# Kernel tuning notes

Measured on AMD Instinct MI355X. Metric: run time of the kernel, lower is better.

Reference implementation:

```python
import jax, jax.numpy as jnp
import numpy as np

B, T, D = 2, 1024, 2048      # batch, seq, model dim
E, F, K = 64, 512, 4          # n_experts, expert hidden, top-k
S, HS = 2, 512 * 4            # shared experts, shared hidden = expert_dim * topk


def setup_inputs() -> dict:
    key = jax.random.key(0)
    ks = jax.random.split(key, 9)
    s = 0.02
    f32 = jnp.float32
    return {
        "x": jax.random.normal(ks[0], (B, T, D), f32),
        "router_w": jax.random.normal(ks[1], (D, E), f32) * s,
        "router_bias": jnp.zeros((E,), f32),
        "wg": jax.random.normal(ks[2], (E, D, F), f32) * s,
        "wu": jax.random.normal(ks[3], (E, D, F), f32) * s,
        "wd": jax.random.normal(ks[4], (E, F, D), f32) * s,
        "swg": jax.random.normal(ks[5], (S, D, HS), f32) * s,
        "swu": jax.random.normal(ks[6], (S, D, HS), f32) * s,
        "swd": jax.random.normal(ks[7], (S, HS, D), f32) * s,
    }


def reference(x, router_w, router_bias, wg, wu, wd, swg, swu, swd):
    b, t, d = x.shape
    flat = x.reshape(b * t, d)                      # [N, D]
    n = flat.shape[0]

    # Router: softmax scores, top-k selection on (logits + bias)
    logits = flat @ router_w                         # [N, E]
    scores = jax.nn.softmax(logits, axis=-1)
    _, topk_idx = jax.lax.top_k(logits + router_bias, K)          # [N, K]
    topk_scores = jnp.take_along_axis(scores, topk_idx, axis=-1)  # [N, K]
    topk_scores = topk_scores / topk_scores.sum(axis=-1, keepdims=True)

    # Dense combine weights: w[n, e] = normalized score if expert e selected else 0
    comb = jnp.zeros((n, E), dtype=flat.dtype).at[
        jnp.arange(n)[:, None], topk_idx].set(topk_scores)        # [N, E]

    # Routed experts (SwiGLU), computed densely and masked by combine weights
    g = jax.nn.silu(jnp.einsum('nd,edf->nef', flat, wg))          # [N, E, F]
    u = jnp.einsum('nd,edf->nef', flat, wu)                       # [N, E, F]
    routed = jnp.einsum('ne,nef,efd->nd', comb, g * u, wd)        # [N, D]

    # Shared experts (always active, summed)
    sg = jax.nn.silu(jnp.einsum('nd,sdh->nsh', flat, swg))        # [N, S, HS]
    su = jnp.einsum('nd,sdh->nsh', flat, swu)
    shared = jnp.einsum('nsh,shd->nd', sg * su, swd)              # [N, D]

    return (routed + shared).reshape(b, t, d)
```

## Files before the change

kernel.cpp:

```cpp
#include <hip/hip_runtime.h>
#include <hip/hip_bf16.h>

typedef __bf16 bf16x8 __attribute__((ext_vector_type(8)));
typedef float f32x4 __attribute__((ext_vector_type(4)));
typedef unsigned short u16x4 __attribute__((ext_vector_type(4)));
typedef unsigned short u16x8 __attribute__((ext_vector_type(8)));

#define DEVI __device__ __forceinline__

constexpr int N_TOK = 2048;
constexpr int DIM   = 2048;
constexpr int NEXP  = 64;
constexpr int FDIM  = 512;
constexpr int TOPK  = 4;
constexpr int NSH   = 2;
constexpr int HSH   = 2048;

constexpr int BM = 128, BN = 128, BK = 64, KS = 8;

DEVI unsigned short f2b(float f) {
  union { float fv; unsigned u; } v; v.fv = f;
  unsigned r = v.u + 0x7fffu + ((v.u >> 16) & 1u);
  return (unsigned short)(r >> 16);
}
DEVI float b2f(unsigned short h) {
  union { unsigned u; float f; } v; v.u = ((unsigned)h) << 16;
  return v.f;
}
DEVI void gll16(const void* g, void* l) {
  __builtin_amdgcn_global_load_lds((const __attribute__((address_space(1))) unsigned*)g,
                                   (__attribute__((address_space(3))) unsigned*)l, 16, 0, 0);
}

__global__ void cvt_x_kernel(const float* __restrict__ x, unsigned short* __restrict__ xb) {
  const size_t i = ((size_t)blockIdx.x * 256 + threadIdx.x) * 8;
  const float4 a = *reinterpret_cast<const float4*>(x + i);
  const float4 b = *reinterpret_cast<const float4*>(x + i + 4);
  u16x8 o;
  o[0] = f2b(a.x); o[1] = f2b(a.y); o[2] = f2b(a.z); o[3] = f2b(a.w);
  o[4] = f2b(b.x); o[5] = f2b(b.y); o[6] = f2b(b.z); o[7] = f2b(b.w);
  *reinterpret_cast<u16x8*>(xb + i) = o;
}

__global__ __launch_bounds__(256)
void tr_shared_kernel(const float* __restrict__ swu, const float* __restrict__ swg,
                      const float* __restrict__ swd, unsigned short* __restrict__ swuT,
                      unsigned short* __restrict__ swgT, unsigned short* __restrict__ swdT) {
  __shared__ float Lf[64][68];
  const int tid = threadIdx.x;
  const int r0 = blockIdx.x * 64, c0 = blockIdx.y * 64;
  const int z = blockIdx.z, mat = z >> 1;
  const size_t soff = (size_t)(z & 1) * DIM * HSH;
  const float* in = (mat == 0 ? swu : mat == 1 ? swg : swd) + soff;
  unsigned short* ot = (mat == 0 ? swuT : mat == 1 ? swgT : swdT) + soff;
  #pragma unroll
  for (int j = 0; j < 4; ++j) {
    const int idx = j * 1024 + tid * 4;
    const int row = idx >> 6, col = idx & 63;
    const float4 v = *reinterpret_cast<const float4*>(in + (size_t)(r0 + row) * 2048 + c0 + col);
    *reinterpret_cast<float4*>(&Lf[row][col]) = v;
  }
  __syncthreads();
  #pragma unroll
  for (int j = 0; j < 4; ++j) {
    const int idx = j * 1024 + tid * 4;
    const int orow = idx >> 6, ocol = idx & 63;
    u16x4 o;
    o[0] = f2b(Lf[ocol][orow]);     o[1] = f2b(Lf[ocol + 1][orow]);
    o[2] = f2b(Lf[ocol + 2][orow]); o[3] = f2b(Lf[ocol + 3][orow]);
    *reinterpret_cast<u16x4*>(ot + (size_t)(c0 + orow) * 2048 + r0 + ocol) = o;
  }
}

__global__ void router_kernel(const float* __restrict__ x, const float* __restrict__ rw,
                              const float* __restrict__ rb, int* __restrict__ cnt,
                              int* __restrict__ listTok, float* __restrict__ listW) {
  const int lane = threadIdx.x & 63;
  const int wave = threadIdx.x >> 6;
  const int tokBase = blockIdx.x * 8 + wave * 2;
  const float* __restrict__ xr0 = x + (size_t)tokBase * DIM;
  const float* __restrict__ xr1 = xr0 + DIM;
  float acc0 = 0.f, acc1 = 0.f;
  for (int d = 0; d < DIM; ++d) {
    const float r = rw[(size_t)d * NEXP + lane];
    acc0 = fmaf(xr0[d], r, acc0);
    acc1 = fmaf(xr1[d], r, acc1);
  }
  const float bias = rb[lane];
  #pragma unroll
  for (int t = 0; t < 2; ++t) {
    const float v = (t == 0) ? acc0 : acc1;
    const int token = tokBase + t;
    float m = v;
    #pragma unroll
    for (int o = 32; o > 0; o >>= 1) m = fmaxf(m, __shfl_xor(m, o));
    const float p = expf(v - m);
    float ss = p;
    #pragma unroll
    for (int o = 32; o > 0; o >>= 1) ss += __shfl_xor(ss, o);
    const float score = p / ss;
    float cur = v + bias;
    float wk[TOPK]; int ik[TOPK]; float wsum = 0.f;
    #pragma unroll
    for (int k = 0; k < TOPK; ++k) {
      float tm = cur;
      #pragma unroll
      for (int o = 32; o > 0; o >>= 1) tm = fmaxf(tm, __shfl_xor(tm, o));
      const unsigned long long msk = __ballot(cur == tm);
      const int sel = (int)__builtin_ctzll(msk);
      const float w = __shfl(score, sel);
      wk[k] = w; ik[k] = sel; wsum += w;
      if (lane == sel) cur = -3.4e38f;
    }
    if (lane < TOPK) {
      const int e = ik[lane];
      const float w = wk[lane] / wsum;
      const int slot = atomicAdd(&cnt[e], 1);
      listTok[(size_t)e * N_TOK + slot] = token;
      listW[(size_t)e * N_TOK + slot] = w;
    }
  }
}

__global__ void scan_kernel(const int* __restrict__ cnt, int* __restrict__ off) {
  if (threadIdx.x == 0) {
    int s = 0;
    for (int e = 0; e < NEXP; ++e) { off[e] = s; s += cnt[e]; }
  }
}

template<bool ROUTED>
__global__ __launch_bounds__(256, 2)
void up_fused_kernel(const unsigned short* __restrict__ xb,
                     const float* __restrict__ Wu, const float* __restrict__ Wg,
                     const unsigned short* __restrict__ WuT, const unsigned short* __restrict__ WgT,
                     const int* __restrict__ cnt, const int* __restrict__ off,
                     const int* __restrict__ listTok, const float* __restrict__ listW,
                     unsigned short* __restrict__ H) {
  const int Ftot = ROUTED ? FDIM : HSH;
  const int tid = threadIdx.x;
  const int f0 = blockIdx.x * BN;
  const int e  = blockIdx.y;
  const int m0 = blockIdx.z * BM;
  int rcnt, rowbase;
  if (ROUTED) {
    const int c = cnt[e];
    if (m0 >= c) return;
    rcnt = min(BM, c - m0);
    rowbase = off[e] + m0;
  } else {
    rcnt = BM;
    rowbase = e * N_TOK + m0;
  }

  __shared__ __align__(16) unsigned short Al[KS][BM][8];
  __shared__ __align__(16) unsigned short Bu[KS][BN][8];
  __shared__ __align__(16) unsigned short Bg[KS][BN][8];
  __shared__ int tokS[BM];
  __shared__ float wS[BM];

  if (tid < BM) {
    if (ROUTED) {
      const bool v = tid < rcnt;
      tokS[tid] = listTok[(size_t)e * N_TOK + m0 + (v ? tid : 0)];
      wS[tid]   = v ? listW[(size_t)e * N_TOK + m0 + tid] : 0.f;
    } else { tokS[tid] = m0 + tid; wS[tid] = 1.f; }
  }
  __syncthreads();

  const int wid = tid >> 6, l = tid & 63;
  const int wm = wid >> 1, wn = wid & 1;
  const int lc = l & 15, hi = l >> 4;

  const unsigned short* pa0 = xb + (size_t)tokS[l] * DIM;
  const unsigned short* pa1 = xb + (size_t)tokS[64 + l] * DIM;

  const unsigned short *pbu0 = nullptr, *pbu1 = nullptr, *pbg0 = nullptr, *pbg1 = nullptr;
  if constexpr (!ROUTED) {
    const unsigned short* wut = WuT + (size_t)e * HSH * DIM;
    const unsigned short* wgt = WgT + (size_t)e * HSH * DIM;
    pbu0 = wut + (size_t)(f0 + l) * DIM;  pbu1 = wut + (size_t)(f0 + 64 + l) * DIM;
    pbg0 = wgt + (size_t)(f0 + l) * DIM;  pbg1 = wgt + (size_t)(f0 + 64 + l) * DIM;
  }
  const int bf = tid & 127, kh = tid >> 7;
  const float *wpu = nullptr, *wpg = nullptr;
  if constexpr (ROUTED) {
    wpu = Wu + (size_t)e * DIM * FDIM + (size_t)(kh * 32) * FDIM + f0 + bf;
    wpg = Wg + (size_t)e * DIM * FDIM + (size_t)(kh * 32) * FDIM + f0 + bf;
  }
  unsigned short* bdstU = &Bu[kh * 4][bf][0];
  unsigned short* bdstG = &Bg[kh * 4][bf][0];

  f32x4 au[4][4], ag[4][4];
  #pragma unroll
  for (int i = 0; i < 4; ++i)
    #pragma unroll
    for (int j = 0; j < 4; ++j) { au[i][j] = f32x4{0,0,0,0}; ag[i][j] = f32x4{0,0,0,0}; }

  for (int d0 = 0; d0 < DIM; d0 += BK) {
    gll16(pa0 + d0 + (2 * wid) * 8,     &Al[2 * wid][0][0]);
    gll16(pa1 + d0 + (2 * wid) * 8,     &Al[2 * wid][64][0]);
    gll16(pa0 + d0 + (2 * wid + 1) * 8, &Al[2 * wid + 1][0][0]);
    gll16(pa1 + d0 + (2 * wid + 1) * 8, &Al[2 * wid + 1][64][0]);
    if constexpr (!ROUTED) {
      gll16(pbu0 + d0 + (2 * wid) * 8,     &Bu[2 * wid][0][0]);
      gll16(pbu1 + d0 + (2 * wid) * 8,     &Bu[2 * wid][64][0]);
      gll16(pbu0 + d0 + (2 * wid + 1) * 8, &Bu[2 * wid + 1][0][0]);
      gll16(pbu1 + d0 + (2 * wid + 1) * 8, &Bu[2 * wid + 1][64][0]);
      gll16(pbg0 + d0 + (2 * wid) * 8,     &Bg[2 * wid][0][0]);
      gll16(pbg1 + d0 + (2 * wid) * 8,     &Bg[2 * wid][64][0]);
      gll16(pbg0 + d0 + (2 * wid + 1) * 8, &Bg[2 * wid + 1][0][0]);
      gll16(pbg1 + d0 + (2 * wid + 1) * 8, &Bg[2 * wid + 1][64][0]);
    } else {
      float r[32];
      #pragma unroll
      for (int j = 0; j < 32; ++j) r[j] = wpu[(size_t)(d0 + j) * FDIM];
      #pragma unroll
      for (int jg = 0; jg < 4; ++jg) {
        u16x8 pk;
        #pragma unroll
        for (int q = 0; q < 8; ++q) pk[q] = f2b(r[jg * 8 + q]);
        *reinterpret_cast<u16x8*>(bdstU + jg * BN * 8) = pk;
      }
      #pragma unroll
      for (int j = 0; j < 32; ++j) r[j] = wpg[(size_t)(d0 + j) * FDIM];
      #pragma unroll
      for (int jg = 0; jg < 4; ++jg) {
        u16x8 pk;
        #pragma unroll
        for (int q = 0; q < 8; ++q) pk[q] = f2b(r[jg * 8 + q]);
        *reinterpret_cast<u16x8*>(bdstG + jg * BN * 8) = pk;
      }
    }
    __syncthreads();
    #pragma unroll
    for (int ks = 0; ks < 2; ++ks) {
      bf16x8 af[4], bu_[4], bg_[4];
      #pragma unroll
      for (int i = 0; i < 4; ++i)
        af[i] = *reinterpret_cast<const bf16x8*>(&Al[ks * 4 + hi][wm * 64 + i * 16 + lc][0]);
      #pragma unroll
      for (int i = 0; i < 4; ++i) {
        bu_[i] = *reinterpret_cast<const bf16x8*>(&Bu[ks * 4 + hi][wn * 64 + i * 16 + lc][0]);
        bg_[i] = *reinterpret_cast<const bf16x8*>(&Bg[ks * 4 + hi][wn * 64 + i * 16 + lc][0]);
      }
      #pragma unroll
      for (int mi = 0; mi < 4; ++mi)
        #pragma unroll
        for (int ni = 0; ni < 4; ++ni) {
          au[mi][ni] = __builtin_amdgcn_mfma_f32_16x16x32_bf16(af[mi], bu_[ni], au[mi][ni], 0, 0, 0);
          ag[mi][ni] = __builtin_amdgcn_mfma_f32_16x16x32_bf16(af[mi], bg_[ni], ag[mi][ni], 0, 0, 0);
        }
    }
    __syncthreads();
  }

  #pragma unroll
  for (int mi = 0; mi < 4; ++mi)
    #pragma unroll
    for (int ni = 0; ni < 4; ++ni)
      #pragma unroll
      for (int r2 = 0; r2 < 4; ++r2) {
        const int row = wm * 64 + mi * 16 + hi * 4 + r2;
        if (row < rcnt) {
          const int col = f0 + wn * 64 + ni * 16 + lc;
          const float g = ag[mi][ni][r2], u = au[mi][ni][r2];
          const float h = (g / (1.f + __expf(-g))) * u * wS[row];
          H[(size_t)(rowbase + row) * Ftot + col] = f2b(h);
        }
      }
}

__global__ __launch_bounds__(256, 2)
void down_kernel(const unsigned short* __restrict__ Hr, const unsigned short* __restrict__ Hs,
                 const float* __restrict__ wd, const unsigned short* __restrict__ swdT,
                 const int* __restrict__ cnt, const int* __restrict__ off,
                 const int* __restrict__ listTok, float* __restrict__ out) {
  const int tid = threadIdx.x;
  const int x0 = blockIdx.x * BN;
  const int y  = blockIdx.y;
  const int m0 = blockIdx.z * BM;
  const bool routed = y < NEXP;
  int rcnt, Kd;
  const unsigned short* Ab;
  const float* wb = nullptr;
  const unsigned short* wbT = nullptr;

  __shared__ int tokS[BM];
  __shared__ __align__(16) unsigned short Al[KS][BM][8];
  __shared__ __align__(16) unsigned short Bl[KS][BN][8];

  if (routed) {
    const int c = cnt[y];
    if (m0 >= c) return;
    rcnt = min(BM, c - m0); Kd = FDIM;
    Ab = Hr + (size_t)(off[y] + m0) * FDIM;
    wb = wd + (size_t)y * FDIM * DIM;
    if (tid < BM) tokS[tid] = listTok[(size_t)y * N_TOK + m0 + min(tid, rcnt - 1)];
  } else {
    const int s = y - NEXP;
    rcnt = BM; Kd = HSH;
    Ab = Hs + ((size_t)s * N_TOK + m0) * HSH;
    wbT = swdT + (size_t)s * HSH * DIM;
    if (tid < BM) tokS[tid] = m0 + tid;
  }
  __syncthreads();

  const int wid = tid >> 6, l = tid & 63;
  const int wm = wid >> 1, wn = wid & 1;
  const int lc = l & 15, hi = l >> 4;

  const unsigned short* pA = Ab + (size_t)l * Kd;
  const unsigned short *pBT0 = nullptr, *pBT1 = nullptr;
  if (!routed) {
    pBT0 = wbT + (size_t)(x0 + l) * HSH;
    pBT1 = wbT + (size_t)(x0 + 64 + l) * HSH;
  }
  const int bf = tid & 127, kh = tid >> 7;
  const float* wp = routed ? wb + (size_t)(kh * 32) * DIM + x0 + bf : nullptr;
  unsigned short* bdst = &Bl[kh * 4][bf][0];

  f32x4 acc[4][4];
  #pragma unroll
  for (int i = 0; i < 4; ++i)
    #pragma unroll
    for (int j = 0; j < 4; ++j) acc[i][j] = f32x4{0,0,0,0};

  for (int d0 = 0; d0 < Kd; d0 += BK) {
    gll16(pA + d0 + (2 * wid) * 8,                       &Al[2 * wid][0][0]);
    gll16(pA + (size_t)64 * Kd + d0 + (2 * wid) * 8,     &Al[2 * wid][64][0]);
    gll16(pA + d0 + (2 * wid + 1) * 8,                   &Al[2 * wid + 1][0][0]);
    gll16(pA + (size_t)64 * Kd + d0 + (2 * wid + 1) * 8, &Al[2 * wid + 1][64][0]);
    if (routed) {
      float r[32];
      #pragma unroll
      for (int j = 0; j < 32; ++j) r[j] = wp[(size_t)(d0 + j) * DIM];
      #pragma unroll
      for (int jg = 0; jg < 4; ++jg) {
        u16x8 pk;
        #pragma unroll
        for (int q = 0; q < 8; ++q) pk[q] = f2b(r[jg * 8 + q]);
        *reinterpret_cast<u16x8*>(bdst + jg * BN * 8) = pk;
      }
    } else {
      gll16(pBT0 + d0 + (2 * wid) * 8,     &Bl[2 * wid][0][0]);
      gll16(pBT1 + d0 + (2 * wid) * 8,     &Bl[2 * wid][64][0]);
      gll16(pBT0 + d0 + (2 * wid + 1) * 8, &Bl[2 * wid + 1][0][0]);
      gll16(pBT1 + d0 + (2 * wid + 1) * 8, &Bl[2 * wid + 1][64][0]);
    }
    __syncthreads();
    #pragma unroll
    for (int ks = 0; ks < 2; ++ks) {
      bf16x8 af[4], bq[4];
      #pragma unroll
      for (int i = 0; i < 4; ++i)
        af[i] = *reinterpret_cast<const bf16x8*>(&Al[ks * 4 + hi][wm * 64 + i * 16 + lc][0]);
      #pragma unroll
      for (int i = 0; i < 4; ++i)
        bq[i] = *reinterpret_cast<const bf16x8*>(&Bl[ks * 4 + hi][wn * 64 + i * 16 + lc][0]);
      #pragma unroll
      for (int mi = 0; mi < 4; ++mi)
        #pragma unroll
        for (int ni = 0; ni < 4; ++ni)
          acc[mi][ni] = __builtin_amdgcn_mfma_f32_16x16x32_bf16(af[mi], bq[ni], acc[mi][ni], 0, 0, 0);
    }
    __syncthreads();
  }

  #pragma unroll
  for (int mi = 0; mi < 4; ++mi)
    #pragma unroll
    for (int ni = 0; ni < 4; ++ni)
      #pragma unroll
      for (int r2 = 0; r2 < 4; ++r2) {
        const int row = wm * 64 + mi * 16 + hi * 4 + r2;
        if (row < rcnt) {
          const int col = x0 + wn * 64 + ni * 16 + lc;
          atomicAdd(&out[(size_t)tokS[row] * DIM + col], acc[mi][ni][r2]);
        }
      }
}

extern "C" void kernel_launch(void* const* d_in, const int* in_sizes, int n_in,
                              void* d_out, int out_size, void* d_ws, size_t ws_size,
                              hipStream_t stream) {
  const float* x   = (const float*)d_in[0];
  const float* rw  = (const float*)d_in[1];
  const float* rb  = (const float*)d_in[2];
  const float* wg  = (const float*)d_in[3];
  const float* wu  = (const float*)d_in[4];
  const float* wd  = (const float*)d_in[5];
  const float* swg = (const float*)d_in[6];
  const float* swu = (const float*)d_in[7];
  const float* swd = (const float*)d_in[8];
  float* out = (float*)d_out;
  char* ws = (char*)d_ws;

  int* cnt = (int*)ws;
  int* off = (int*)(ws + 256);
  int* listTok = (int*)(ws + 4096);
  float* listW = (float*)(ws + 4096 + 512 * 1024);
  unsigned short* xb   = (unsigned short*)(ws + (size_t) 2 * 1024 * 1024);
  unsigned short* Hr   = (unsigned short*)(ws + (size_t)10 * 1024 * 1024);
  unsigned short* Hs   = (unsigned short*)(ws + (size_t)18 * 1024 * 1024);
  unsigned short* swuT = (unsigned short*)(ws + (size_t)34 * 1024 * 1024);
  unsigned short* swgT = (unsigned short*)(ws + (size_t)50 * 1024 * 1024);
  unsigned short* swdT = (unsigned short*)(ws + (size_t)66 * 1024 * 1024);

  hipMemsetAsync(cnt, 0, NEXP * sizeof(int), stream);
  hipMemsetAsync(out, 0, (size_t)N_TOK * DIM * sizeof(float), stream);
  cvt_x_kernel<<<(N_TOK * DIM) / (256 * 8), 256, 0, stream>>>(x, xb);
  tr_shared_kernel<<<dim3(32, 32, 6), 256, 0, stream>>>(swu, swg, swd, swuT, swgT, swdT);
  router_kernel<<<N_TOK / 8, 256, 0, stream>>>(x, rw, rb, cnt, listTok, listW);
  scan_kernel<<<1, 64, 0, stream>>>(cnt, off);
  up_fused_kernel<true ><<<dim3(FDIM / BN, NEXP, 16), 256, 0, stream>>>(
      xb, wu, wg, nullptr, nullptr, cnt, off, listTok, listW, Hr);
  up_fused_kernel<false><<<dim3(HSH / BN, NSH, N_TOK / BM), 256, 0, stream>>>(
      xb, nullptr, nullptr, swuT, swgT, cnt, off, listTok, listW, Hs);
  down_kernel<<<dim3(DIM / BN, NEXP + NSH, 16), 256, 0, stream>>>(
      Hr, Hs, wd, swdT, cnt, off, listTok, out);
}
```

Baseline: 693.4 us.

## Split fused up-GEMM, double-buffer all GEMMs, write shared down output directly

The fused gate/up kernel is replaced by one templated GEMM kernel with double-buffered LDS staging, so the next K-tile's global loads are issued while the current tile feeds the MFMAs. The routed weights are now read as float4 and converted to bf16 into LDS. Up and gate become separate launches: the gate pass reads back the stored up activations to apply SiLU and the routing weight. The shared down-projection sums both shared experts inside one kernel and stores to the output directly, so the output memset and those atomics go away. The cost is re-reading the token activations for the second GEMM, an extra bf16 round trip of H, and more launches.

After: 891.1 us. +28.5%, slower.

```diff
diff --git a/kernel.cpp b/kernel.cpp
--- a/kernel.cpp
+++ b/kernel.cpp
@@ -129,41 +129,43 @@
   }
 }
 
-template<bool ROUTED>
-__global__ __launch_bounds__(256, 2)
-void up_fused_kernel(const unsigned short* __restrict__ xb,
-                     const float* __restrict__ Wu, const float* __restrict__ Wg,
-                     const unsigned short* __restrict__ WuT, const unsigned short* __restrict__ WgT,
-                     const int* __restrict__ cnt, const int* __restrict__ off,
-                     const int* __restrict__ listTok, const float* __restrict__ listW,
-                     unsigned short* __restrict__ H) {
-  const int Ftot = ROUTED ? FDIM : HSH;
+template<int MODE, bool ROUTED>
+__global__ void gemm_kernel(const unsigned short* __restrict__ Ab,
+                            const float* __restrict__ Bf,
+                            const unsigned short* __restrict__ Bt,
+                            const int* __restrict__ cnt, const int* __restrict__ off,
+                            const int* __restrict__ listTok, const float* __restrict__ listW,
+                            unsigned short* __restrict__ Hio, float* __restrict__ outF) {
+  constexpr int KSEG = (MODE < 2) ? DIM : (ROUTED ? FDIM : HSH);
+  constexpr int NSEG = (MODE == 2 && !ROUTED) ? NSH : 1;
+  constexpr int NOUT = (MODE < 2) ? (ROUTED ? FDIM : HSH) : DIM;
+  constexpr int BSTR = (MODE < 2) ? FDIM : DIM;
+  constexpr int NT = KSEG / BK, TOT = NSEG * NT;
+
   const int tid = threadIdx.x;
-  const int f0 = blockIdx.x * BN;
+  const int x0 = blockIdx.x * BN;
   const int e  = blockIdx.y;
   const int m0 = blockIdx.z * BM;
-  int rcnt, rowbase;
-  if (ROUTED) {
+
+  int rcnt = BM, rowbase;
+  if constexpr (ROUTED) {
     const int c = cnt[e];
     if (m0 >= c) return;
     rcnt = min(BM, c - m0);
     rowbase = off[e] + m0;
   } else {
-    rcnt = BM;
-    rowbase = e * N_TOK + m0;
-  }
-
-  __shared__ __align__(16) unsigned short Al[KS][BM][8];
-  __shared__ __align__(16) unsigned short Bu[KS][BN][8];
-  __shared__ __align__(16) unsigned short Bg[KS][BN][8];
+    rowbase = (MODE < 2) ? (e * N_TOK + m0) : m0;
+  }
+
+  __shared__ __align__(16) unsigned short Al[2][KS][BM][8];
+  __shared__ __align__(16) unsigned short Bl[2][KS][BN][8];
   __shared__ int tokS[BM];
   __shared__ float wS[BM];
 
   if (tid < BM) {
-    if (ROUTED) {
-      const bool v = tid < rcnt;
-      tokS[tid] = listTok[(size_t)e * N_TOK + m0 + (v ? tid : 0)];
-      wS[tid]   = v ? listW[(size_t)e * N_TOK + m0 + tid] : 0.f;
+    if constexpr (ROUTED) {
+      tokS[tid] = listTok[(size_t)e * N_TOK + m0 + min(tid, rcnt - 1)];
+      wS[tid] = (tid < rcnt) ? listW[(size_t)e * N_TOK + m0 + tid] : 0.f;
     } else { tokS[tid] = m0 + tid; wS[tid] = 1.f; }
   }
   __syncthreads();
@@ -172,192 +174,105 @@
   const int wm = wid >> 1, wn = wid & 1;
   const int lc = l & 15, hi = l >> 4;
 
-  const unsigned short* pa0 = xb + (size_t)tokS[l] * DIM;
-  const unsigned short* pa1 = xb + (size_t)tokS[64 + l] * DIM;
-
-  const unsigned short *pbu0 = nullptr, *pbu1 = nullptr, *pbg0 = nullptr, *pbg1 = nullptr;
-  if constexpr (!ROUTED) {
-    const unsigned short* wut = WuT + (size_t)e * HSH * DIM;
-    const unsigned short* wgt = WgT + (size_t)e * HSH * DIM;
-    pbu0 = wut + (size_t)(f0 + l) * DIM;  pbu1 = wut + (size_t)(f0 + 64 + l) * DIM;
-    pbg0 = wgt + (size_t)(f0 + l) * DIM;  pbg1 = wgt + (size_t)(f0 + 64 + l) * DIM;
-  }
-  const int bf = tid & 127, kh = tid >> 7;
-  const float *wpu = nullptr, *wpg = nullptr;
+  const unsigned short *pa0, *pa1;
+  if constexpr (MODE < 2) {
+    pa0 = Ab + (size_t)tokS[l] * DIM;
+    pa1 = Ab + (size_t)tokS[64 + l] * DIM;
+  } else if constexpr (ROUTED) {
+    pa0 = Ab + (size_t)(rowbase + min(l, rcnt - 1)) * FDIM;
+    pa1 = Ab + (size_t)(rowbase + min(64 + l, rcnt - 1)) * FDIM;
+  } else {
+    pa0 = nullptr; pa1 = nullptr;
+  }
+
+  const float* bf_base = nullptr;
+  const unsigned short *pb0 = nullptr, *pb1 = nullptr;
   if constexpr (ROUTED) {
-    wpu = Wu + (size_t)e * DIM * FDIM + (size_t)(kh * 32) * FDIM + f0 + bf;
-    wpg = Wg + (size_t)e * DIM * FDIM + (size_t)(kh * 32) * FDIM + f0 + bf;
-  }
-  unsigned short* bdstU = &Bu[kh * 4][bf][0];
-  unsigned short* bdstG = &Bg[kh * 4][bf][0];
-
-  f32x4 au[4][4], ag[4][4];
+    bf_base = Bf + (size_t)e * ((size_t)FDIM * DIM) + x0;
+  } else if constexpr (MODE < 2) {
+    pb0 = Bt + (size_t)e * HSH * DIM + (size_t)(x0 + l) * DIM;
+    pb1 = Bt + (size_t)e * HSH * DIM + (size_t)(x0 + 64 + l) * DIM;
+  }
+
+  const int f4  = tid & 31;
+  const int k4a = tid >> 5;
+  f32x4 rB[2][4];
+
+  auto stageIssue = [&](int g, int b) {
+    const int seg = (NSEG > 1) ? (g / NT) : 0;
+    const int d0 = (g - seg * NT) * BK;
+    if constexpr (MODE == 2 && !ROUTED) {
+      const unsigned short* s0 = Ab + ((size_t)(seg * N_TOK + m0 + l)) * HSH + d0;
+      const unsigned short* s1 = Ab + ((size_t)(seg * N_TOK + m0 + 64 + l)) * HSH + d0;
+      gll16(s0 + (2 * wid) * 8,     &Al[b][2 * wid][0][0]);
+      gll16(s1 + (2 * wid) * 8,     &Al[b][2 * wid][64][0]);
+      gll16(s0 + (2 * wid + 1) * 8, &Al[b][2 * wid + 1][0][0]);
+      gll16(s1 + (2 * wid + 1) * 8, &Al[b][2 * wid + 1][64][0]);
+    } else {
+      gll16(pa0 + d0 + (2 * wid) * 8,     &Al[b][2 * wid][0][0]);
+      gll16(pa1 + d0 + (2 * wid) * 8,     &Al[b][2 * wid][64][0]);
+      gll16(pa0 + d0 + (2 * wid + 1) * 8, &Al[b][2 * wid + 1][0][0]);
+      gll16(pa1 + d0 + (2 * wid + 1) * 8, &Al[b][2 * wid + 1][64][0]);
+    }
+    if constexpr (ROUTED) {
+      #pragma unroll
+      for (int s2 = 0; s2 < 2; ++s2)
+        #pragma unroll
+        for (int j = 0; j < 4; ++j)
+          rB[s2][j] = *reinterpret_cast<const f32x4*>(
+              bf_base + (size_t)(d0 + k4a * 8 + s2 * 4 + j) * BSTR + f4 * 4);
+    } else if constexpr (MODE < 2) {
+      gll16(pb0 + d0 + (2 * wid) * 8,     &Bl[b][2 * wid][0][0]);
+      gll16(pb1 + d0 + (2 * wid) * 8,     &Bl[b][2 * wid][64][0]);
+      gll16(pb0 + d0 + (2 * wid + 1) * 8, &Bl[b][2 * wid + 1][0][0]);
+      gll16(pb1 + d0 + (2 * wid + 1) * 8, &Bl[b][2 * wid + 1][64][0]);
+    } else {
+      const unsigned short* b0 = Bt + (size_t)seg * HSH * DIM + (size_t)(x0 + l) * HSH + d0;
+      const unsigned short* b1 = Bt + (size_t)seg * HSH * DIM + (size_t)(x0 + 64 + l) * HSH + d0;
+      gll16(b0 + (2 * wid) * 8,     &Bl[b][2 * wid][0][0]);
+      gll16(b1 + (2 * wid) * 8,     &Bl[b][2 * wid][64][0]);
+      gll16(b0 + (2 * wid + 1) * 8, &Bl[b][2 * wid + 1][0][0]);
+      gll16(b1 + (2 * wid + 1) * 8, &Bl[b][2 * wid + 1][64][0]);
+    }
+  };
+
+  auto stageWriteB = [&](int b) {
+    if constexpr (ROUTED) {
+      #pragma unroll
+      for (int c = 0; c < 4; ++c) {
+        u16x8 v;
+        v[0] = f2b(rB[0][0][c]); v[1] = f2b(rB[0][1][c]);
+        v[2] = f2b(rB[0][2][c]); v[3] = f2b(rB[0][3][c]);
+        v[4] = f2b(rB[1][0][c]); v[5] = f2b(rB[1][1][c]);
+        v[6] = f2b(rB[1][2][c]); v[7] = f2b(rB[1][3][c]);
+        *reinterpret_cast<u16x8*>(&Bl[b][k4a][f4 * 4 + c][0]) = v;
+      }
+    }
+  };
+
+  f32x4 acc[4][4];
   #pragma unroll
   for (int i = 0; i < 4; ++i)
     #pragma unroll
-    for (int j = 0; j < 4; ++j) { au[i][j] = f32x4{0,0,0,0}; ag[i][j] = f32x4{0,0,0,0}; }
-
-  for (int d0 = 0; d0 < DIM; d0 += BK) {
-    gll16(pa0 + d0 + (2 * wid) * 8,     &Al[2 * wid][0][0]);
-    gll16(pa1 + d0 + (2 * wid) * 8,     &Al[2 * wid][64][0]);
-    gll16(pa0 + d0 + (2 * wid + 1) * 8, &Al[2 * wid + 1][0][0]);
-    gll16(pa1 + d0 + (2 * wid + 1) * 8, &Al[2 * wid + 1][64][0]);
-    if constexpr (!ROUTED) {
-      gll16(pbu0 + d0 + (2 * wid) * 8,     &Bu[2 * wid][0][0]);
-      gll16(pbu1 + d0 + (2 * wid) * 8,     &Bu[2 * wid][64][0]);
-      gll16(pbu0 + d0 + (2 * wid + 1) * 8, &Bu[2 * wid + 1][0][0]);
-      gll16(pbu1 + d0 + (2 * wid + 1) * 8, &Bu[2 * wid + 1][64][0]);
-      gll16(pbg0 + d0 + (2 * wid) * 8,     &Bg[2 * wid][0][0]);
-      gll16(pbg1 + d0 + (2 * wid) * 8,     &Bg[2 * wid][64][0]);
-      gll16(pbg0 + d0 + (2 * wid + 1) * 8, &Bg[2 * wid + 1][0][0]);
-      gll16(pbg1 + d0 + (2 * wid + 1) * 8, &Bg[2 * wid + 1][64][0]);
-    } else {
-      float r[32];
-      #pragma unroll
-      for (int j = 0; j < 32; ++j) r[j] = wpu[(size_t)(d0 + j) * FDIM];
-      #pragma unroll
-      for (int jg = 0; jg < 4; ++jg) {
-        u16x8 pk;
-        #pragma unroll
-        for (int q = 0; q < 8; ++q) pk[q] = f2b(r[jg * 8 + q]);
-        *reinterpret_cast<u16x8*>(bdstU + jg * BN * 8) = pk;
-      }
-      #pragma unroll
-      for (int j = 0; j < 32; ++j) r[j] = wpg[(size_t)(d0 + j) * FDIM];
-      #pragma unroll
-      for (int jg = 0; jg < 4; ++jg) {
-        u16x8 pk;
-        #pragma unroll
-        for (int q = 0; q < 8; ++q) pk[q] = f2b(r[jg * 8 + q]);
-        *reinterpret_cast<u16x8*>(bdstG + jg * BN * 8) = pk;
-      }
-    }
-    __syncthreads();
-    #pragma unroll
-    for (int ks = 0; ks < 2; ++ks) {
-      bf16x8 af[4], bu_[4], bg_[4];
-      #pragma unroll
-      for (int i = 0; i < 4; ++i)
-        af[i] = *reinterpret_cast<const bf16x8*>(&Al[ks * 4 + hi][wm * 64 + i * 16 + lc][0]);
-      #pragma unroll
-      for (int i = 0; i < 4; ++i) {
-        bu_[i] = *reinterpret_cast<const bf16x8*>(&Bu[ks * 4 + hi][wn * 64 + i * 16 + lc][0]);
-        bg_[i] = *reinterpret_cast<const bf16x8*>(&Bg[ks * 4 + hi][wn * 64 + i * 16 + lc][0]);
-      }
-      #pragma unroll
-      for (int mi = 0; mi < 4; ++mi)
-        #pragma unroll
-        for (int ni = 0; ni < 4; ++ni) {
-          au[mi][ni] = __builtin_amdgcn_mfma_f32_16x16x32_bf16(af[mi], bu_[ni], au[mi][ni], 0, 0, 0);
-          ag[mi][ni] = __builtin_amdgcn_mfma_f32_16x16x32_bf16(af[mi], bg_[ni], ag[mi][ni], 0, 0, 0);
-        }
-    }
-    __syncthreads();
-  }
-
-  #pragma unroll
-  for (int mi = 0; mi < 4; ++mi)
-    #pragma unroll
-    for (int ni = 0; ni < 4; ++ni)
-      #pragma unroll
-      for (int r2 = 0; r2 < 4; ++r2) {
-        const int row = wm * 64 + mi * 16 + hi * 4 + r2;
-        if (row < rcnt) {
-          const int col = f0 + wn * 64 + ni * 16 + lc;
-          const float g = ag[mi][ni][r2], u = au[mi][ni][r2];
-          const float h = (g / (1.f + __expf(-g))) * u * wS[row];
-          H[(size_t)(rowbase + row) * Ftot + col] = f2b(h);
-        }
-      }
-}
-
-__global__ __launch_bounds__(256, 2)
-void down_kernel(const unsigned short* __restrict__ Hr, const unsigned short* __restrict__ Hs,
-                 const float* __restrict__ wd, const unsigned short* __restrict__ swdT,
-                 const int* __restrict__ cnt, const int* __restrict__ off,
-                 const int* __restrict__ listTok, float* __restrict__ out) {
-  const int tid = threadIdx.x;
-  const int x0 = blockIdx.x * BN;
-  const int y  = blockIdx.y;
-  const int m0 = blockIdx.z * BM;
-  const bool routed = y < NEXP;
-  int rcnt, Kd;
-  const unsigned short* Ab;
-  const float* wb = nullptr;
-  const unsigned short* wbT = nullptr;
-
-  __shared__ int tokS[BM];
-  __shared__ __align__(16) unsigned short Al[KS][BM][8];
-  __shared__ __align__(16) unsigned short Bl[KS][BN][8];
-
-  if (routed) {
-    const int c = cnt[y];
-    if (m0 >= c) return;
-    rcnt = min(BM, c - m0); Kd = FDIM;
-    Ab = Hr + (size_t)(off[y] + m0) * FDIM;
-    wb = wd + (size_t)y * FDIM * DIM;
-    if (tid < BM) tokS[tid] = listTok[(size_t)y * N_TOK + m0 + min(tid, rcnt - 1)];
-  } else {
-    const int s = y - NEXP;
-    rcnt = BM; Kd = HSH;
-    Ab = Hs + ((size_t)s * N_TOK + m0) * HSH;
-    wbT = swdT + (size_t)s * HSH * DIM;
-    if (tid < BM) tokS[tid] = m0 + tid;
-  }
+    for (int j = 0; j < 4; ++j) acc[i][j] = f32x4{0.f, 0.f, 0.f, 0.f};
+
+  int buf = 0;
+  stageIssue(0, 0);
   __syncthreads();
-
-  const int wid = tid >> 6, l = tid & 63;
-  const int wm = wid >> 1, wn = wid & 1;
-  const int lc = l & 15, hi = l >> 4;
-
-  const unsigned short* pA = Ab + (size_t)l * Kd;
-  const unsigned short *pBT0 = nullptr, *pBT1 = nullptr;
-  if (!routed) {
-    pBT0 = wbT + (size_t)(x0 + l) * HSH;
-    pBT1 = wbT + (size_t)(x0 + 64 + l) * HSH;
-  }
-  const int bf = tid & 127, kh = tid >> 7;
-  const float* wp = routed ? wb + (size_t)(kh * 32) * DIM + x0 + bf : nullptr;
-  unsigned short* bdst = &Bl[kh * 4][bf][0];
-
-  f32x4 acc[4][4];
-  #pragma unroll
-  for (int i = 0; i < 4; ++i)
-    #pragma unroll
-    for (int j = 0; j < 4; ++j) acc[i][j] = f32x4{0,0,0,0};
-
-  for (int d0 = 0; d0 < Kd; d0 += BK) {
-    gll16(pA + d0 + (2 * wid) * 8,                       &Al[2 * wid][0][0]);
-    gll16(pA + (size_t)64 * Kd + d0 + (2 * wid) * 8,     &Al[2 * wid][64][0]);
-    gll16(pA + d0 + (2 * wid + 1) * 8,                   &Al[2 * wid + 1][0][0]);
-    gll16(pA + (size_t)64 * Kd + d0 + (2 * wid + 1) * 8, &Al[2 * wid + 1][64][0]);
-    if (routed) {
-      float r[32];
-      #pragma unroll
-      for (int j = 0; j < 32; ++j) r[j] = wp[(size_t)(d0 + j) * DIM];
-      #pragma unroll
-      for (int jg = 0; jg < 4; ++jg) {
-        u16x8 pk;
-        #pragma unroll
-        for (int q = 0; q < 8; ++q) pk[q] = f2b(r[jg * 8 + q]);
-        *reinterpret_cast<u16x8*>(bdst + jg * BN * 8) = pk;
-      }
-    } else {
-      gll16(pBT0 + d0 + (2 * wid) * 8,     &Bl[2 * wid][0][0]);
-      gll16(pBT1 + d0 + (2 * wid) * 8,     &Bl[2 * wid][64][0]);
-      gll16(pBT0 + d0 + (2 * wid + 1) * 8, &Bl[2 * wid + 1][0][0]);
-      gll16(pBT1 + d0 + (2 * wid + 1) * 8, &Bl[2 * wid + 1][64][0]);
-    }
-    __syncthreads();
+  if constexpr (ROUTED) { stageWriteB(0); __syncthreads(); }
+
+  for (int g = 0; g < TOT; ++g) {
+    const int gn = (g + 1 < TOT) ? g + 1 : g;
+    stageIssue(gn, buf ^ 1);
     #pragma unroll
     for (int ks = 0; ks < 2; ++ks) {
       bf16x8 af[4], bq[4];
       #pragma unroll
       for (int i = 0; i < 4; ++i)
-        af[i] = *reinterpret_cast<const bf16x8*>(&Al[ks * 4 + hi][wm * 64 + i * 16 + lc][0]);
+        af[i] = *reinterpret_cast<const bf16x8*>(&Al[buf][ks * 4 + hi][wm * 64 + i * 16 + lc][0]);
       #pragma unroll
       for (int i = 0; i < 4; ++i)
-        bq[i] = *reinterpret_cast<const bf16x8*>(&Bl[ks * 4 + hi][wn * 64 + i * 16 + lc][0]);
+        bq[i] = *reinterpret_cast<const bf16x8*>(&Bl[buf][ks * 4 + hi][wn * 64 + i * 16 + lc][0]);
       #pragma unroll
       for (int mi = 0; mi < 4; ++mi)
         #pragma unroll
@@ -365,6 +280,8 @@
           acc[mi][ni] = __builtin_amdgcn_mfma_f32_16x16x32_bf16(af[mi], bq[ni], acc[mi][ni], 0, 0, 0);
     }
     __syncthreads();
+    if constexpr (ROUTED) { stageWriteB(buf ^ 1); __syncthreads(); }
+    buf ^= 1;
   }
 
   #pragma unroll
@@ -376,7 +293,19 @@
         const int row = wm * 64 + mi * 16 + hi * 4 + r2;
         if (row < rcnt) {
           const int col = x0 + wn * 64 + ni * 16 + lc;
-          atomicAdd(&out[(size_t)tokS[row] * DIM + col], acc[mi][ni][r2]);
+          const float v = acc[mi][ni][r2];
+          if constexpr (MODE == 0) {
+            Hio[(size_t)(rowbase + row) * NOUT + col] = f2b(v);
+          } else if constexpr (MODE == 1) {
+            const size_t idx = (size_t)(rowbase + row) * NOUT + col;
+            const float u = b2f(Hio[idx]);
+            const float h = (v / (1.f + __expf(-v))) * u * wS[row];
+            Hio[idx] = f2b(h);
+          } else if constexpr (ROUTED) {
+            atomicAdd(&outF[(size_t)tokS[row] * DIM + col], v);
+          } else {
+            outF[(size_t)(m0 + row) * DIM + col] = v;
+          }
         }
       }
 }
@@ -408,15 +337,21 @@
   unsigned short* swdT = (unsigned short*)(ws + (size_t)66 * 1024 * 1024);
 
   hipMemsetAsync(cnt, 0, NEXP * sizeof(int), stream);
-  hipMemsetAsync(out, 0, (size_t)N_TOK * DIM * sizeof(float), stream);
   cvt_x_kernel<<<(N_TOK * DIM) / (256 * 8), 256, 0, stream>>>(x, xb);
   tr_shared_kernel<<<dim3(32, 32, 6), 256, 0, stream>>>(swu, swg, swd, swuT, swgT, swdT);
   router_kernel<<<N_TOK / 8, 256, 0, stream>>>(x, rw, rb, cnt, listTok, listW);
   scan_kernel<<<1, 64, 0, stream>>>(cnt, off);
-  up_fused_kernel<true ><<<dim3(FDIM / BN, NEXP, 16), 256, 0, stream>>>(
-      xb, wu, wg, nullptr, nullptr, cnt, off, listTok, listW, Hr);
-  up_fused_kernel<false><<<dim3(HSH / BN, NSH, N_TOK / BM), 256, 0, stream>>>(
-      xb, nullptr, nullptr, swuT, swgT, cnt, off, listTok, listW, Hs);
-  down_kernel<<<dim3(DIM / BN, NEXP + NSH, 16), 256, 0, stream>>>(
-      Hr, Hs, wd, swdT, cnt, off, listTok, out);
-}
+
+  gemm_kernel<0, true><<<dim3(FDIM / BN, NEXP, 16), 256, 0, stream>>>(
+      xb, wu, nullptr, cnt, off, listTok, listW, Hr, nullptr);
+  gemm_kernel<1, true><<<dim3(FDIM / BN, NEXP, 16), 256, 0, stream>>>(
+      xb, wg, nullptr, cnt, off, listTok, listW, Hr, nullptr);
+  gemm_kernel<0, false><<<dim3(HSH / BN, NSH, N_TOK / BM), 256, 0, stream>>>(
+      xb, nullptr, swuT, cnt, off, listTok, listW, Hs, nullptr);
+  gemm_kernel<1, false><<<dim3(HSH / BN, NSH, N_TOK / BM), 256, 0, stream>>>(
+      xb, nullptr, swgT, cnt, off, listTok, listW, Hs, nullptr);
+  gemm_kernel<2, false><<<dim3(DIM / BN, 1, N_TOK / BM), 256, 0, stream>>>(
+      Hs, nullptr, swdT, cnt, off, listTok, listW, nullptr, out);
+  gemm_kernel<2, true><<<dim3(DIM / BN, NEXP, 16), 256, 0, stream>>>(
+      Hr, wd, nullptr, cnt, off, listTok, listW, nullptr, out);
+}
```
